# Kernel tuning notes

Hardware: AMD Instinct MI355X
Metric: run time of the kernel (lower is better)

Reference implementation:

```python
import jax, jax.numpy as jnp
import numpy as np

B, C, H, W = 16, 64, 512, 512

def setup_inputs() -> dict:
    key = jax.random.key(0)
    x = jax.random.normal(key, (B, C, H, W), dtype=jnp.float32)
    return {"x": x}

def reference(x):
    # x: [B, C, H, W] with even H, W. Haar subbands per 2x2 block, matching
    # torch cross-correlation with stride 2 and the given kernels.
    Bx, Cx, Hx, Wx = x.shape
    xb = x.reshape(Bx, Cx, Hx // 2, 2, Wx // 2, 2)
    a = xb[:, :, :, 0, :, 0]  # top-left
    b = xb[:, :, :, 0, :, 1]  # top-right
    c = xb[:, :, :, 1, :, 0]  # bottom-left
    d = xb[:, :, :, 1, :, 1]  # bottom-right
    half = jnp.float32(0.5)
    out_LL = (a + b + c + d) * half
    out_LH = (a - b + c - d) * half
    out_HL = (a + b - c - d) * half
    out_HH = (a - b - c + d) * half
    return (out_LL, out_LH, out_HL, out_HH)
```

## Files before the change

kernel.cpp:

```cpp
#include <hip/hip_runtime.h>
#include <hip/hip_bf16.h>


#define B_ 16
#define C_ 64
#define H_ 512
#define W_ 512
#define HO (H_/2)
#define WO (W_/2)
#define NPLANE (B_*C_*HO*WO)
#define W2 (WO/2)
#define NWORK (B_*C_*HO*W2)

__global__ __launch_bounds__(256) void haar_kernel(const float* __restrict__ x,
                                                   float* __restrict__ out) {
    const long long stride = (long long)gridDim.x * blockDim.x;
    for (long long idx = (long long)blockIdx.x * blockDim.x + threadIdx.x;
         idx < (long long)NWORK; idx += stride) {
        const int w2 = (int)(idx & (W2 - 1));
        long long rest = idx >> 7;
        const int h = (int)(rest & (HO - 1));
        const long long bc = rest >> 8;

        const long long in_base = bc * (long long)(H_ * W_) + (long long)(2 * h) * W_ + 4 * w2;
        const float4 r0 = *reinterpret_cast<const float4*>(x + in_base);
        const float4 r1 = *reinterpret_cast<const float4*>(x + in_base + W_);

        const float a0 = r0.x, b0 = r0.y, a1 = r0.z, b1 = r0.w;
        const float c0 = r1.x, d0 = r1.y, c1 = r1.z, d1 = r1.w;

        float2 ll, lh, hl, hh;
        ll.x = (a0 + b0 + c0 + d0) * 0.5f;
        ll.y = (a1 + b1 + c1 + d1) * 0.5f;
        lh.x = (a0 - b0 + c0 - d0) * 0.5f;
        lh.y = (a1 - b1 + c1 - d1) * 0.5f;
        hl.x = (a0 + b0 - c0 - d0) * 0.5f;
        hl.y = (a1 + b1 - c1 - d1) * 0.5f;
        hh.x = (a0 - b0 - c0 + d0) * 0.5f;
        hh.y = (a1 - b1 - c1 + d1) * 0.5f;

        const long long out_base = bc * (long long)(HO * WO) + (long long)h * WO + 2 * w2;
        *reinterpret_cast<float2*>(out + out_base)               = ll;
        *reinterpret_cast<float2*>(out + out_base + 1LL*NPLANE)  = lh;
        *reinterpret_cast<float2*>(out + out_base + 2LL*NPLANE)  = hl;
        *reinterpret_cast<float2*>(out + out_base + 3LL*NPLANE)  = hh;
    }
}

extern "C" void kernel_launch(void* const* d_in, const int* in_sizes, int n_in,
                              void* d_out, int out_size, void* d_ws, size_t ws_size,
                              hipStream_t stream) {
    const float* x = (const float*)d_in[0];
    float* out = (float*)d_out;
    const int block = 256;
    const int grid = 2048;
    haar_kernel<<<grid, block, 0, stream>>>(x, out);
}
```

Before: 461.9 us.

## Stage subband outputs through LDS to emit 16-byte coalesced stores

Restructures work so each block handles 8 input rows (4 output rows) of one plane per iteration. Each wave computes two output rows' worth of all four subbands, writes them to shared memory, and after a barrier each wave stores one subband with 16-byte vector writes instead of 8-byte float2 writes. This is meant to improve store efficiency on a purely bandwidth-bound kernel, at the cost of two block barriers per iteration and extra LDS traffic.

```diff
diff --git a/kernel.cpp b/kernel.cpp
--- a/kernel.cpp
+++ b/kernel.cpp
@@ -9,41 +9,72 @@
 #define HO (H_/2)
 #define WO (W_/2)
 #define NPLANE (B_*C_*HO*WO)
-#define W2 (WO/2)
-#define NWORK (B_*C_*HO*W2)
+#define NITER 32
+
+typedef float f32x4 __attribute__((ext_vector_type(4)));
+typedef float f32x2 __attribute__((ext_vector_type(2)));
 
 __global__ __launch_bounds__(256) void haar_kernel(const float* __restrict__ x,
                                                    float* __restrict__ out) {
-    const long long stride = (long long)gridDim.x * blockDim.x;
-    for (long long idx = (long long)blockIdx.x * blockDim.x + threadIdx.x;
-         idx < (long long)NWORK; idx += stride) {
-        const int w2 = (int)(idx & (W2 - 1));
-        long long rest = idx >> 7;
-        const int h = (int)(rest & (HO - 1));
-        const long long bc = rest >> 8;
+    __shared__ float lds[4][4][256];
+    const int w    = threadIdx.x >> 6;
+    const int lane = threadIdx.x & 63;
 
-        const long long in_base = bc * (long long)(H_ * W_) + (long long)(2 * h) * W_ + 4 * w2;
-        const float4 r0 = *reinterpret_cast<const float4*>(x + in_base);
-        const float4 r1 = *reinterpret_cast<const float4*>(x + in_base + W_);
+    for (int j = 0; j < NITER; ++j) {
+        const int t  = j * 2048 + (int)blockIdx.x;
+        const int bc = t >> 6;
+        const int h4 = t & 63;
 
-        const float a0 = r0.x, b0 = r0.y, a1 = r0.z, b1 = r0.w;
-        const float c0 = r1.x, d0 = r1.y, c1 = r1.z, d1 = r1.w;
+        const float* in_row = x + (size_t)bc * (H_ * W_)
+                                + (size_t)(h4 * 8 + 2 * w) * W_ + 4 * lane;
+        const f32x4 r0a = *reinterpret_cast<const f32x4*>(in_row);
+        const f32x4 r0b = *reinterpret_cast<const f32x4*>(in_row + 256);
+        const f32x4 r1a = *reinterpret_cast<const f32x4*>(in_row + W_);
+        const f32x4 r1b = *reinterpret_cast<const f32x4*>(in_row + W_ + 256);
 
-        float2 ll, lh, hl, hh;
-        ll.x = (a0 + b0 + c0 + d0) * 0.5f;
-        ll.y = (a1 + b1 + c1 + d1) * 0.5f;
-        lh.x = (a0 - b0 + c0 - d0) * 0.5f;
-        lh.y = (a1 - b1 + c1 - d1) * 0.5f;
-        hl.x = (a0 + b0 - c0 - d0) * 0.5f;
-        hl.y = (a1 + b1 - c1 - d1) * 0.5f;
-        hh.x = (a0 - b0 - c0 + d0) * 0.5f;
-        hh.y = (a1 - b1 - c1 + d1) * 0.5f;
+        f32x2 ll_a, lh_a, hl_a, hh_a, ll_b, lh_b, hl_b, hh_b;
+        {
+            float p0 = r0a[0] + r0a[1], q0 = r0a[0] - r0a[1];
+            float r0 = r1a[0] + r1a[1], s0 = r1a[0] - r1a[1];
+            ll_a[0] = (p0 + r0) * 0.5f; hl_a[0] = (p0 - r0) * 0.5f;
+            lh_a[0] = (q0 + s0) * 0.5f; hh_a[0] = (q0 - s0) * 0.5f;
+            float p1 = r0a[2] + r0a[3], q1 = r0a[2] - r0a[3];
+            float r1 = r1a[2] + r1a[3], s1 = r1a[2] - r1a[3];
+            ll_a[1] = (p1 + r1) * 0.5f; hl_a[1] = (p1 - r1) * 0.5f;
+            lh_a[1] = (q1 + s1) * 0.5f; hh_a[1] = (q1 - s1) * 0.5f;
+        }
+        {
+            float p0 = r0b[0] + r0b[1], q0 = r0b[0] - r0b[1];
+            float r0 = r1b[0] + r1b[1], s0 = r1b[0] - r1b[1];
+            ll_b[0] = (p0 + r0) * 0.5f; hl_b[0] = (p0 - r0) * 0.5f;
+            lh_b[0] = (q0 + s0) * 0.5f; hh_b[0] = (q0 - s0) * 0.5f;
+            float p1 = r0b[2] + r0b[3], q1 = r0b[2] - r0b[3];
+            float r1 = r1b[2] + r1b[3], s1 = r1b[2] - r1b[3];
+            ll_b[1] = (p1 + r1) * 0.5f; hl_b[1] = (p1 - r1) * 0.5f;
+            lh_b[1] = (q1 + s1) * 0.5f; hh_b[1] = (q1 - s1) * 0.5f;
+        }
 
-        const long long out_base = bc * (long long)(HO * WO) + (long long)h * WO + 2 * w2;
-        *reinterpret_cast<float2*>(out + out_base)               = ll;
-        *reinterpret_cast<float2*>(out + out_base + 1LL*NPLANE)  = lh;
-        *reinterpret_cast<float2*>(out + out_base + 2LL*NPLANE)  = hl;
-        *reinterpret_cast<float2*>(out + out_base + 3LL*NPLANE)  = hh;
+        *reinterpret_cast<f32x2*>(&lds[w][0][2 * lane])       = ll_a;
+        *reinterpret_cast<f32x2*>(&lds[w][0][128 + 2 * lane]) = ll_b;
+        *reinterpret_cast<f32x2*>(&lds[w][1][2 * lane])       = lh_a;
+        *reinterpret_cast<f32x2*>(&lds[w][1][128 + 2 * lane]) = lh_b;
+        *reinterpret_cast<f32x2*>(&lds[w][2][2 * lane])       = hl_a;
+        *reinterpret_cast<f32x2*>(&lds[w][2][128 + 2 * lane]) = hl_b;
+        *reinterpret_cast<f32x2*>(&lds[w][3][2 * lane])       = hh_a;
+        *reinterpret_cast<f32x2*>(&lds[w][3][128 + 2 * lane]) = hh_b;
+
+        __syncthreads();
+
+        float* plane_base = out + (size_t)w * NPLANE + (size_t)bc * (HO * WO)
+                                + (size_t)(h4 * 4) * WO + 4 * lane;
+#pragma unroll
+        for (int s = 0; s < 4; ++s) {
+            const int r = (w + s) & 3;
+            const f32x4 v = *reinterpret_cast<const f32x4*>(&lds[r][w][4 * lane]);
+            *reinterpret_cast<f32x4*>(plane_base + (size_t)r * WO) = v;
+        }
+
+        __syncthreads();
     }
 }
 
@@ -52,7 +83,5 @@
                               hipStream_t stream) {
     const float* x = (const float*)d_in[0];
     float* out = (float*)d_out;
-    const int block = 256;
-    const int grid = 2048;
-    haar_kernel<<<grid, block, 0, stream>>>(x, out);
+    haar_kernel<<<2048, 256, 0, stream>>>(x, out);
 }
```

After: 421.4 us. 1.1x faster.
